# Kernel tuning notes

Measured on AMD Instinct MI355X. Metric: run time of the kernel, lower is better.

Reference implementation:

```python
import jax, jax.numpy as jnp
import numpy as np

D = 2048
H = 16
DK = D // H
B = 2
S = 2048


def setup_inputs() -> dict:
    key = jax.random.key(0)
    ks = jax.random.split(key, 11)
    s = 1.0 / np.sqrt(D)
    inp = {
        "q": jax.random.normal(ks[0], (B, S, D), jnp.float32),
        "k": jax.random.normal(ks[1], (B, S, D), jnp.float32),
        "v": jax.random.normal(ks[2], (B, S, D), jnp.float32),
        "mask": 0,
        "Wq": jax.random.normal(ks[3], (D, D), jnp.float32) * s,
        "bq": jax.random.normal(ks[4], (D,), jnp.float32) * s,
        "Wk": jax.random.normal(ks[5], (D, D), jnp.float32) * s,
        "bk": jax.random.normal(ks[6], (D,), jnp.float32) * s,
        "Wv": jax.random.normal(ks[7], (D, D), jnp.float32) * s,
        "bv": jax.random.normal(ks[8], (D,), jnp.float32) * s,
        "Wo": jax.random.normal(ks[9], (D, D), jnp.float32) * s,
        "bo": jax.random.normal(ks[10], (D,), jnp.float32) * s,
    }
    return inp


def reference(q, k, v, mask, Wq, bq, Wk, bk, Wv, bv, Wo, bo):
    # Linear projections (torch Linear: x @ W.T + b)
    query = q @ Wq.T + bq  # [B,S,D]
    key_ = k @ Wk.T + bk
    value = v @ Wv.T + bv
    # split heads -> [B,S,H,DK]
    query = query.reshape(B, S, H, DK)
    key_ = key_.reshape(B, S, H, DK)
    value = value.reshape(B, S, H, DK)
    # scores [B,H,Sq,Sk]
    scores = jnp.einsum('nqhd,nkhd->nhqk', query, key_)
    if mask:
        # faithful to source: fill where triu(ones, diag=1) == 0 (lower tri incl diag)
        tri = jnp.triu(jnp.ones((S, S), jnp.float32), k=1)
        scores = jnp.where(tri == 0, jnp.float32(-1e20), scores)
    attn = jax.nn.softmax(scores / np.sqrt(DK), axis=3)
    # dropout=0.0 -> identity
    out = jnp.einsum('nhql,nlhd->nqhd', attn, value).reshape(B, S, D)
    return out @ Wo.T + bo
```

## Files before the change

### kernel.cpp

```cpp
#include <hip/hip_runtime.h>
#include <math.h>

typedef unsigned short u16;
typedef u16 u16x8 __attribute__((ext_vector_type(8)));
typedef u16 u16x4 __attribute__((ext_vector_type(4)));
typedef short s16x8 __attribute__((ext_vector_type(8)));
typedef short s16x4 __attribute__((ext_vector_type(4)));
typedef float f32x4 __attribute__((ext_vector_type(4)));

static constexpr int B_ = 2;
static constexpr int S_ = 2048;
static constexpr int D_ = 2048;
static constexpr int H_ = 16;
static constexpr int DK = 128;
static constexpr long long BSD = (long long)B_ * S_ * D_;
static constexpr long long DD  = (long long)D_ * D_;

#if __has_builtin(__builtin_amdgcn_mfma_f32_16x16x32_bf16)
#define HAVE_MFMA32 1
#else
#define HAVE_MFMA32 0
#endif
#if __has_builtin(__builtin_amdgcn_mfma_f32_16x16x16bf16_1k)
#define HAVE_MFMA16 1
#else
#define HAVE_MFMA16 0
#endif

__device__ __forceinline__ u16 f2bf(float f) {
    union { float f; unsigned u; } cv; cv.f = f;
    unsigned u = cv.u;
    return (u16)((u + 0x7fffu + ((u >> 16) & 1u)) >> 16);
}

__device__ __forceinline__ unsigned pack2bf(float a, float b) {
    union { float f; unsigned u; } x, y; x.f = a; y.f = b;
    return ((y.u + 0x8000u) & 0xffff0000u) | ((x.u + 0x8000u) >> 16);
}

__device__ __forceinline__ f32x4 mfma32(f32x4 c, u16x8 a, u16x8 b) {
#if HAVE_MFMA32
    return __builtin_amdgcn_mfma_f32_16x16x32_bf16((s16x8)a, (s16x8)b, c, 0, 0, 0);
#else
    asm volatile("v_mfma_f32_16x16x32_bf16 %0, %1, %2, %0" : "+v"(c) : "v"(a), "v"(b));
    return c;
#endif
}
__device__ __forceinline__ f32x4 mfma16(f32x4 c, u16x4 a, u16x4 b) {
#if HAVE_MFMA16
    return __builtin_amdgcn_mfma_f32_16x16x16bf16_1k((s16x4)a, (s16x4)b, c, 0, 0, 0);
#else
    asm volatile("v_mfma_f32_16x16x16_bf16 %0, %1, %2, %0" : "+v"(c) : "v"(a), "v"(b));
    return c;
#endif
}
__device__ __forceinline__ void fenceB() {
#if !HAVE_MFMA32 || !HAVE_MFMA16
    asm volatile("s_nop 7\ns_nop 7" :::);
#endif
}

__device__ __forceinline__ void glds16(const u16* g, u16* l) {
    __builtin_amdgcn_global_load_lds(
        (const __attribute__((address_space(1))) unsigned int*)g,
        (__attribute__((address_space(3))) unsigned int*)l, 16, 0, 0);
}

__device__ __forceinline__ float fexp2(float x) {
#if __has_builtin(__builtin_amdgcn_exp2f)
    return __builtin_amdgcn_exp2f(x);
#else
    return exp2f(x);
#endif
}

__device__ __forceinline__ void cfence() { asm volatile("" ::: "memory"); }
__device__ __forceinline__ void barrier8() {
    cfence();
    __builtin_amdgcn_s_barrier();
    cfence();
}
#define LGKM0() do { asm volatile("s_waitcnt lgkmcnt(0)" ::: "memory"); \
                     __builtin_amdgcn_sched_barrier(0); } while (0)
#define VMC(N)  asm volatile("s_waitcnt vmcnt(" #N ")" ::: "memory")

struct CastArgs {
    const float* src[7];
    u16* dst[7];
    int start[8];
};
__global__ __launch_bounds__(256) void cast_all(CastArgs a) {
    int g = blockIdx.x * 256 + threadIdx.x;
    if (g >= a.start[7]) return;
    int seg = 0;
#pragma unroll
    for (int i = 1; i < 7; ++i) seg += (g >= a.start[i]) ? 1 : 0;
    int idx = g - a.start[seg];
    float4 f = ((const float4*)a.src[seg])[idx];
    ushort4 o;
    o.x = f2bf(f.x); o.y = f2bf(f.y); o.z = f2bf(f.z); o.w = f2bf(f.w);
    ((ushort4*)a.dst[seg])[idx] = o;
}

#define GEMM_K64_LOOP(Aptr, Bptr)                                                   \
    for (int k0 = 0; k0 < D_; k0 += 64) {                                           \
        __syncthreads();                                                            \
        _Pragma("unroll")                                                           \
        for (int s = 0; s < 4; ++s) {                                               \
            int slot = s * 256 + t;                                                 \
            int row = slot >> 3;                                                    \
            int c = (t & 7) ^ (row & 7);                                            \
            glds16(Aptr + (m0 + row) * D_ + k0 + c * 8, &As[slot * 8]);             \
        }                                                                           \
        _Pragma("unroll")                                                           \
        for (int s = 0; s < 4; ++s) {                                               \
            int slot = s * 256 + t;                                                 \
            int row = slot >> 3;                                                    \
            int c = (t & 7) ^ (row & 7);                                            \
            glds16(Bptr + (n0 + row) * D_ + k0 + c * 8, &Bs[slot * 8]);             \
        }                                                                           \
        __syncthreads();                                                            \
        u16x8 af[4][2], bf[4][2];                                                   \
        _Pragma("unroll")                                                           \
        for (int i = 0; i < 4; ++i) {                                               \
            int row = wm + i * 16 + l16;                                            \
            _Pragma("unroll")                                                       \
            for (int kk = 0; kk < 2; ++kk)                                          \
                af[i][kk] = *(const u16x8*)(&As[row * 64 +                          \
                                (((kk * 4 + quad) ^ (row & 7)) * 8)]);              \
        }                                                                           \
        _Pragma("unroll")                                                           \
        for (int j = 0; j < 4; ++j) {                                               \
            int row = wn + j * 16 + l16;                                            \
            _Pragma("unroll")                                                       \
            for (int kk = 0; kk < 2; ++kk)                                          \
                bf[j][kk] = *(const u16x8*)(&Bs[row * 64 +                          \
                                (((kk * 4 + quad) ^ (row & 7)) * 8)]);              \
        }                                                                           \
        _Pragma("unroll")                                                           \
        for (int kk = 0; kk < 2; ++kk)                                              \
            _Pragma("unroll")                                                       \
            for (int i = 0; i < 4; ++i)                                             \
                _Pragma("unroll")                                                   \
                for (int j = 0; j < 4; ++j)                                         \
                    acc[i][j] = mfma32(acc[i][j], af[i][kk], bf[j][kk]);            \
    }

struct QkvArgs {
    const u16* X[3];
    const u16* W[3];
    const float* bias[3];
    u16* outQ;
    u16* outK;
    u16* outVt;
    float scaleQ;
};

#define STAGE_HALF(LDS, GBASE)                                                      \
    _Pragma("unroll")                                                               \
    for (int jj = 0; jj < 2; ++jj) {                                                \
        int slot = jj * 512 + t;                                                    \
        int row = slot >> 3, c = slot & 7;                                          \
        glds16((GBASE) + (long long)row * D_ + ((c ^ (row & 7)) * 8),               \
               (LDS) + slot * 8);                                                   \
    }

#define RD_A(QM, LDSA)                                                              \
    _Pragma("unroll")                                                               \
    for (int i2 = 0; i2 < 4; ++i2) {                                                \
        int row = wm128 + (QM) * 64 + i2 * 16 + l16;                                \
        _Pragma("unroll")                                                           \
        for (int kk = 0; kk < 2; ++kk)                                              \
            af[(QM) * 4 + i2][kk] = *(const u16x8*)(&(LDSA)[row * 64 +              \
                                (((kk * 4 + quad) ^ (row & 7)) * 8)]);              \
    }

#define RD_B(QN, LDSB)                                                              \
    _Pragma("unroll")                                                               \
    for (int j2 = 0; j2 < 2; ++j2) {                                                \
        int row = wn64 + (QN) * 32 + j2 * 16 + l16;                                 \
        _Pragma("unroll")                                                           \
        for (int kk = 0; kk < 2; ++kk)                                              \
            bf[j2][kk] = *(const u16x8*)(&(LDSB)[row * 64 +                         \
                                (((kk * 4 + quad) ^ (row & 7)) * 8)]);              \
    }

#define MM(QM, QN)                                                                  \
    __builtin_amdgcn_s_setprio(1);                                                  \
    _Pragma("unroll")                                                               \
    for (int kk = 0; kk < 2; ++kk)                                                  \
        _Pragma("unroll")                                                           \
        for (int i2 = 0; i2 < 4; ++i2)                                              \
            _Pragma("unroll")                                                       \
            for (int j2 = 0; j2 < 2; ++j2)                                          \
                acc[(QM) * 4 + i2][(QN) * 2 + j2] =                                 \
                    mfma32(acc[(QM) * 4 + i2][(QN) * 2 + j2],                       \
                           af[(QM) * 4 + i2][kk], bf[j2][kk]);                      \
    __builtin_amdgcn_s_setprio(0);

__global__ __launch_bounds__(512, 2) void qkv_proj8(QkvArgs a) {
    __shared__ u16 SM8[65536];
    u16* const As0 = SM8;
    u16* const As1 = SM8 + 16384;
    u16* const Bs0 = SM8 + 32768;
    u16* const Bs1 = SM8 + 49152;

    const int zsel = blockIdx.z;
    const u16* __restrict__ Ag = a.X[zsel];
    const u16* __restrict__ Bg = a.W[zsel];

    const int t = threadIdx.x;
    const int lane = t & 63;
    const int quad = lane >> 4, l16 = lane & 15;
    const int wave = t >> 6;
    const int wm128 = (wave >> 2) * 128;
    const int wn64  = (wave & 3) * 64;
    const long long m0 = (long long)blockIdx.y * 256;
    const long long n0 = (long long)blockIdx.x * 256;

    f32x4 acc[8][4];
#pragma unroll
    for (int i = 0; i < 8; ++i)
#pragma unroll
        for (int j = 0; j < 4; ++j)
            acc[i][j] = f32x4{0.f, 0.f, 0.f, 0.f};

    u16x8 af[8][2];
    u16x8 bf[2][2];

    STAGE_HALF(As0,         Ag + m0 * D_)
    STAGE_HALF(As0 + 8192,  Ag + (m0 + 128) * D_)
    STAGE_HALF(Bs0,         Bg + n0 * D_)
    STAGE_HALF(Bs0 + 8192,  Bg + (n0 + 128) * D_)
    STAGE_HALF(As1,         Ag + m0 * D_ + 64)
    STAGE_HALF(As1 + 8192,  Ag + (m0 + 128) * D_ + 64)
    VMC(4);
    barrier8();

#pragma unroll 1
    for (int it = 0; it < 16; ++it) {
        const int E = 2 * it;
        const bool more = (it < 15);
        const long long kO  = (long long)(E + 1) * 64;
        const long long kE2 = (long long)(E + 2) * 64;
        const long long kO2 = (long long)(E + 3) * 64;

        RD_A(0, As0) RD_B(0, Bs0)
        STAGE_HALF(Bs1,        Bg + n0 * D_ + kO)
        barrier8(); LGKM0(); MM(0, 0) barrier8();

        RD_A(1, As0) RD_B(1, Bs0)
        STAGE_HALF(Bs1 + 8192, Bg + (n0 + 128) * D_ + kO)
        barrier8(); LGKM0(); MM(0, 1) barrier8();

        RD_B(0, Bs0)
        if (more) { STAGE_HALF(As0,        Ag + m0 * D_ + kE2) }
        barrier8(); LGKM0(); MM(1, 0) barrier8();

        RD_B(1, Bs0)
        if (more) { STAGE_HALF(As0 + 8192, Ag + (m0 + 128) * D_ + kE2) }
        barrier8(); LGKM0(); MM(1, 1)
        if (more) { VMC(4); } else { VMC(0); }
        barrier8();

        RD_A(0, As1) RD_B(0, Bs1)
        if (more) { STAGE_HALF(Bs0,        Bg + n0 * D_ + kE2) }
        barrier8(); LGKM0(); MM(0, 0) barrier8();

        RD_A(1, As1) RD_B(1, Bs1)
        if (more) { STAGE_HALF(Bs0 + 8192, Bg + (n0 + 128) * D_ + kE2) }
        barrier8(); LGKM0(); MM(0, 1) barrier8();

        RD_B(0, Bs1)
        if (more) { STAGE_HALF(As1,        Ag + m0 * D_ + kO2) }
        barrier8(); LGKM0(); MM(1, 0) barrier8();

        RD_B(1, Bs1)
        if (more) { STAGE_HALF(As1 + 8192, Ag + (m0 + 128) * D_ + kO2) }
        barrier8(); LGKM0(); MM(1, 1)
        if (more) { VMC(4); }
        barrier8();
    }
    fenceB();

    float bs[4];
#pragma unroll
    for (int j = 0; j < 4; ++j)
        bs[j] = a.bias[zsel][(int)n0 + wn64 + j * 16 + l16];

    if (zsel < 2) {
        const float scale = (zsel == 0) ? a.scaleQ : 1.0f;
        u16* C = (zsel == 0) ? a.outQ : a.outK;
#pragma unroll
        for (int i = 0; i < 8; ++i)
#pragma unroll
            for (int j = 0; j < 4; ++j)
#pragma unroll
                for (int r = 0; r < 4; ++r) {
                    int row = wm128 + i * 16 + quad * 4 + r;
                    int col = wn64 + j * 16 + l16;
                    SM8[row * 256 + col] = f2bf((acc[i][j][r] + bs[j]) * scale);
                }
        barrier8();
#pragma unroll
        for (int s = 0; s < 16; ++s) {
            int idx = s * 512 + t;
            int row = idx >> 5, c = idx & 31;
            *(u16x8*)(C + (m0 + row) * (long long)D_ + n0 + c * 8) =
                *(const u16x8*)(&SM8[row * 256 + c * 8]);
        }
    } else {
        const int h0 = (int)(n0 >> 7);
        const int bb = (int)(m0 >> 11);
        const int tok0 = (int)(m0 & 2047);
#pragma unroll
        for (int pass = 0; pass < 2; ++pass) {
            barrier8();
            if ((wn64 >> 7) == pass) {
                int cb = wn64 & 127;
#pragma unroll
                for (int i = 0; i < 8; ++i)
#pragma unroll
                    for (int j = 0; j < 4; ++j)
#pragma unroll
                        for (int r = 0; r < 4; ++r) {
                            int row = wm128 + i * 16 + quad * 4 + r;
                            int d = cb + j * 16 + l16;
                            SM8[d * 264 + row] = f2bf(acc[i][j][r] + bs[j]);
                        }
            }
            barrier8();
            u16* vt = a.outVt + (long long)(bb * 16 + h0 + pass) * DK * S_;
#pragma unroll
            for (int s = 0; s < 8; ++s) {
                int idx = s * 512 + t;
                int d = idx >> 5, tc = idx & 31;
                *(u16x8*)(vt + (long long)d * S_ + tok0 + tc * 8) =
                    *(const u16x8*)(&SM8[d * 264 + tc * 8]);
            }
        }
    }
}

__global__ __launch_bounds__(256) void gemm_out(const u16* __restrict__ Ain,
                                                const u16* __restrict__ Bin,
                                                float* __restrict__ C,
                                                const float* __restrict__ bias) {
    __shared__ u16 SM[16384];
    u16* As = SM;
    u16* Bs = SM + 8192;

    const int t = threadIdx.x;
    const int wave = t >> 6, lane = t & 63;
    const int quad = lane >> 4, l16 = lane & 15;
    const int wm = (wave >> 1) * 64;
    const int wn = (wave & 1) * 64;
    const long long m0 = (long long)blockIdx.y * 128;
    const long long n0 = (long long)blockIdx.x * 128;

    f32x4 acc[4][4];
#pragma unroll
    for (int i = 0; i < 4; ++i)
#pragma unroll
        for (int j = 0; j < 4; ++j)
            acc[i][j] = f32x4{0.f, 0.f, 0.f, 0.f};

    GEMM_K64_LOOP(Ain, Bin)

    fenceB();

    float bs[4];
#pragma unroll
    for (int j = 0; j < 4; ++j)
        bs[j] = bias[(int)n0 + wn + j * 16 + l16];

    float* Cf = (float*)SM;
#pragma unroll
    for (int p = 0; p < 2; ++p) {
        __syncthreads();
#pragma unroll
        for (int jj = 0; jj < 2; ++jj) {
            int j = p * 2 + jj;
#pragma unroll
            for (int i = 0; i < 4; ++i)
#pragma unroll
                for (int r = 0; r < 4; ++r) {
                    int row = wm + i * 16 + quad * 4 + r;
                    int lc = (wave & 1) * 32 + jj * 16 + l16;
                    Cf[row * 64 + lc] = acc[i][j][r] + bs[j];
                }
        }
        __syncthreads();
#pragma unroll
        for (int i = 0; i < 8; ++i) {
            int idx = i * 256 + t;
            int row = idx >> 4, c4 = idx & 15;
            f32x4 val = *(const f32x4*)(&Cf[row * 64 + c4 * 4]);
            long long n = n0 + (c4 >> 3) * 64 + p * 32 + (c4 & 7) * 4;
            *(f32x4*)(C + (m0 + row) * (long long)D_ + n) = val;
        }
    }
}

__global__ __launch_bounds__(256, 2) void flash_attn(const u16* __restrict__ Qb,
                                                     const u16* __restrict__ Kb,
                                                     const u16* __restrict__ Vt,
                                                     u16* __restrict__ Ob) {
    __shared__ u16 Ks[2][64 * 128];
    __shared__ u16 Vs[2][128 * 64];

    const int z  = blockIdx.x;
    const int qt = blockIdx.y;
    const int b  = z >> 4, h = z & 15;
    const int t = threadIdx.x, wave = t >> 6, lane = t & 63;
    const int quad = lane >> 4, l16 = lane & 15;

    const u16* kbase = Kb + (long long)(b * S_) * D_ + h * DK;
    const u16* vbase = Vt + (long long)z * DK * S_;

    u16x8 qf[2][4];
    {
        const u16* qbase = Qb + ((long long)(b * S_ + qt * 128 + wave * 32 + l16)) * D_
                              + h * DK + quad * 8;
#pragma unroll
        for (int jq = 0; jq < 2; ++jq)
#pragma unroll
            for (int kk = 0; kk < 4; ++kk)
                qf[jq][kk] = *(const u16x8*)(qbase + (long long)jq * 16 * D_ + kk * 32);
    }

    f32x4 acc_o[2][8];
#pragma unroll
    for (int jq = 0; jq < 2; ++jq)
#pragma unroll
        for (int jd = 0; jd < 8; ++jd)
            acc_o[jq][jd] = f32x4{0.f, 0.f, 0.f, 0.f};
    float l_[2] = {0.f, 0.f};

    u16x8 vreg[4];

    {
#pragma unroll
        for (int i = 0; i < 4; ++i) {
            int slot = i * 256 + t;
            int row = slot >> 3, c16 = slot & 7;
            vreg[i] = *(const u16x8*)(vbase + (long long)row * S_ + c16 * 8);
        }
#pragma unroll
        for (int i = 0; i < 4; ++i) {
            int slot = i * 256 + t;
            int row = slot >> 4;
            int cs = (slot & 15) ^ (row & 7);
            glds16(kbase + (long long)row * D_ + cs * 8, &Ks[0][slot * 8]);
        }
#pragma unroll
        for (int i = 0; i < 4; ++i) {
            int slot = i * 256 + t;
            int row = slot >> 3, c16 = slot & 7;
            int rm = row & 15;
            u16x4 lo = __builtin_shufflevector(vreg[i], vreg[i], 0, 1, 2, 3);
            u16x4 hi = __builtin_shufflevector(vreg[i], vreg[i], 4, 5, 6, 7);
            *(u16x4*)(&Vs[0][row * 64 + (((2 * c16) ^ rm) * 4)]) = lo;
            *(u16x4*)(&Vs[0][row * 64 + (((2 * c16 + 1) ^ rm) * 4)]) = hi;
        }
    }

    for (int kt = 0; kt < S_ / 64; ++kt) {
        __syncthreads();
        const int p = kt & 1;
        const u16* ks = Ks[p];
        const u16* vs = Vs[p];
        const bool pre = (kt + 1) < (S_ / 64);
        if (pre) {
            const u16* vsrc = vbase + (kt + 1) * 64;
#pragma unroll
            for (int i = 0; i < 4; ++i) {
                int slot = i * 256 + t;
                int row = slot >> 3, c16 = slot & 7;
                vreg[i] = *(const u16x8*)(vsrc + (long long)row * S_ + c16 * 8);
            }
            const u16* ksrc = kbase + (long long)(kt + 1) * 64 * D_;
#pragma unroll
            for (int i = 0; i < 4; ++i) {
                int slot = i * 256 + t;
                int row = slot >> 4;
                int cs = (slot & 15) ^ (row & 7);
                glds16(ksrc + (long long)row * D_ + cs * 8, &Ks[p ^ 1][slot * 8]);
            }
        }

        f32x4 st[4][2];
#pragma unroll
        for (int ik = 0; ik < 4; ++ik)
#pragma unroll
            for (int jq = 0; jq < 2; ++jq)
                st[ik][jq] = f32x4{0.f, 0.f, 0.f, 0.f};
#pragma unroll
        for (int kk = 0; kk < 4; ++kk) {
            u16x8 kf[4];
#pragma unroll
            for (int ik = 0; ik < 4; ++ik) {
                int krow = ik * 16 + l16;
                kf[ik] = *(const u16x8*)(&ks[krow * 128 + (((kk * 4 + quad) ^ (l16 & 7)) * 8)]);
            }
#pragma unroll
            for (int ik = 0; ik < 4; ++ik) {
                st[ik][0] = mfma32(st[ik][0], kf[ik], qf[0][kk]);
                st[ik][1] = mfma32(st[ik][1], kf[ik], qf[1][kk]);
            }
        }
        fenceB();

        if (pre) {
#pragma unroll
            for (int i = 0; i < 4; ++i) {
                int slot = i * 256 + t;
                int row = slot >> 3, c16 = slot & 7;
                int rm = row & 15;
                u16x4 lo = __builtin_shufflevector(vreg[i], vreg[i], 0, 1, 2, 3);
                u16x4 hi = __builtin_shufflevector(vreg[i], vreg[i], 4, 5, 6, 7);
                *(u16x4*)(&Vs[p ^ 1][row * 64 + (((2 * c16) ^ rm) * 4)]) = lo;
                *(u16x4*)(&Vs[p ^ 1][row * 64 + (((2 * c16 + 1) ^ rm) * 4)]) = hi;
            }
        }

        u16x4 pf[4][2];
#pragma unroll
        for (int ik = 0; ik < 4; ++ik)
#pragma unroll
            for (int jq = 0; jq < 2; ++jq) {
                float p0 = fexp2(st[ik][jq][0]);
                float p1 = fexp2(st[ik][jq][1]);
                float p2 = fexp2(st[ik][jq][2]);
                float p3 = fexp2(st[ik][jq][3]);
                l_[jq] += (p0 + p1) + (p2 + p3);
                union { u16x4 v; unsigned u[2]; } pk;
                pk.u[0] = pack2bf(p0, p1);
                pk.u[1] = pack2bf(p2, p3);
                pf[ik][jq] = pk.v;
            }

#pragma unroll
        for (int ik = 0; ik < 4; ++ik) {
            const int kc = ik * 4 + quad;
            u16x4 vf[8];
#pragma unroll
            for (int jd = 0; jd < 8; ++jd) {
                int vrow = jd * 16 + l16;
                vf[jd] = *(const u16x4*)(&vs[vrow * 64 + ((kc ^ l16) * 4)]);
            }
#pragma unroll
            for (int jd = 0; jd < 8; ++jd) {
                acc_o[0][jd] = mfma16(acc_o[0][jd], pf[ik][0], vf[jd]);
                acc_o[1][jd] = mfma16(acc_o[1][jd], pf[ik][1], vf[jd]);
            }
        }
        fenceB();
    }

    float lr[2][4];
#pragma unroll
    for (int jq = 0; jq < 2; ++jq) {
        float s = l_[jq];
        s += __shfl_xor(s, 16, 64);
        s += __shfl_xor(s, 32, 64);
        float inv = 1.f / s;
#pragma unroll
        for (int r = 0; r < 4; ++r)
            lr[jq][r] = __shfl(inv, quad * 20 + r, 64);
    }
    u16* OS = (u16*)Ks;
    __syncthreads();
#pragma unroll
    for (int jq = 0; jq < 2; ++jq)
#pragma unroll
        for (int r = 0; r < 4; ++r) {
            int qloc = wave * 32 + jq * 16 + quad * 4 + r;
#pragma unroll
            for (int jd = 0; jd < 8; ++jd)
                OS[qloc * 128 + jd * 16 + l16] = f2bf(acc_o[jq][jd][r] * lr[jq][r]);
        }
    __syncthreads();
    u16* obase = Ob + ((long long)(b * S_ + qt * 128)) * D_ + h * DK;
#pragma unroll
    for (int i = 0; i < 8; ++i) {
        int idx = i * 256 + t;
        int row = idx >> 4, cc = idx & 15;
        *(u16x8*)(obase + (long long)row * D_ + cc * 8) = *(const u16x8*)(&OS[row * 128 + cc * 8]);
    }
}

extern "C" void kernel_launch(void* const* d_in, const int* in_sizes, int n_in,
                              void* d_out, int out_size, void* d_ws, size_t ws_size,
                              hipStream_t stream) {
    const float* q  = (const float*)d_in[0];
    const float* k  = (const float*)d_in[1];
    const float* v  = (const float*)d_in[2];
    const float* Wq = (const float*)d_in[4];
    const float* bq = (const float*)d_in[5];
    const float* Wk = (const float*)d_in[6];
    const float* bk = (const float*)d_in[7];
    const float* Wv = (const float*)d_in[8];
    const float* bv = (const float*)d_in[9];
    const float* Wo = (const float*)d_in[10];
    const float* bo = (const float*)d_in[11];
    float* out = (float*)d_out;

    u16* ws = (u16*)d_ws;
    u16* xq  = ws; ws += BSD;
    u16* xk  = ws; ws += BSD;
    u16* xv  = ws; ws += BSD;
    u16* wqb = ws; ws += DD;
    u16* wkb = ws; ws += DD;
    u16* wvb = ws; ws += DD;
    u16* wob = ws; ws += DD;
    u16* Qb  = ws; ws += BSD;
    u16* Kb  = ws; ws += BSD;
    u16* Vt  = ws; ws += BSD;
    u16* Ob  = ws; ws += BSD;

    const float q_scale = (float)(0.08838834764831845 * 1.4426950408889634);

    {
        CastArgs a;
        const float* srcs[7] = {q, k, v, Wq, Wk, Wv, Wo};
        u16* dsts[7] = {xq, xk, xv, wqb, wkb, wvb, wob};
        int n4s[7] = {(int)(BSD / 4), (int)(BSD / 4), (int)(BSD / 4),
                      (int)(DD / 4), (int)(DD / 4), (int)(DD / 4), (int)(DD / 4)};
        int acc = 0;
        for (int i = 0; i < 7; ++i) { a.src[i] = srcs[i]; a.dst[i] = dsts[i]; a.start[i] = acc; acc += n4s[i]; }
        a.start[7] = acc;
        cast_all<<<(acc + 255) / 256, 256, 0, stream>>>(a);
    }

    {
        QkvArgs a;
        a.X[0] = xq;  a.X[1] = xk;  a.X[2] = xv;
        a.W[0] = wqb; a.W[1] = wkb; a.W[2] = wvb;
        a.bias[0] = bq; a.bias[1] = bk; a.bias[2] = bv;
        a.outQ = Qb; a.outK = Kb; a.outVt = Vt;
        a.scaleQ = q_scale;
        qkv_proj8<<<dim3(D_ / 256, (B_ * S_) / 256, 3), 512, 0, stream>>>(a);
    }

    flash_attn<<<dim3(B_ * H_, S_ / 128), 256, 0, stream>>>(Qb, Kb, Vt, Ob);

    gemm_out<<<dim3(D_ / 128, (B_ * S_) / 128), 256, 0, stream>>>(Ob, wob, out, bo);
}
```

Baseline: 448.8 us.

## Restructure QKV projection into 128x256 tiles with triple-buffered LDS and remapped grid

Replaces the 256x256-tile double-buffered QKV GEMM with a 128x256 tile using a three-slot rotating LDS buffer that stages each K-step's A and B tiles together. The 3D grid becomes a 1D grid of 768 blocks with a custom index swizzle mapping blocks to (z, n, m). Halving the per-block accumulator count lowers register pressure, and the extra blocks give more of them per CU. The aim is better load/compute overlap and occupancy, at the cost of more LDS per block and less data reuse per tile. The V-transpose epilogue is simplified into a single pass.

New measurement: 434.3 us. -3.2%, faster.

```diff
diff --git a/kernel.cpp b/kernel.cpp
--- a/kernel.cpp
+++ b/kernel.cpp
@@ -156,56 +156,50 @@
     float scaleQ;
 };
 
-#define STAGE_HALF(LDS, GBASE)                                                      \
+#define STAGE_U(LDSP, GBASE)                                                        \
     _Pragma("unroll")                                                               \
     for (int jj = 0; jj < 2; ++jj) {                                                \
         int slot = jj * 512 + t;                                                    \
         int row = slot >> 3, c = slot & 7;                                          \
         glds16((GBASE) + (long long)row * D_ + ((c ^ (row & 7)) * 8),               \
-               (LDS) + slot * 8);                                                   \
-    }
-
-#define RD_A(QM, LDSA)                                                              \
+               (LDSP) + slot * 8);                                                  \
+    }
+
+#define RD_K(kk, AsT, BsT)                                                          \
     _Pragma("unroll")                                                               \
     for (int i2 = 0; i2 < 4; ++i2) {                                                \
-        int row = wm128 + (QM) * 64 + i2 * 16 + l16;                                \
-        _Pragma("unroll")                                                           \
-        for (int kk = 0; kk < 2; ++kk)                                              \
-            af[(QM) * 4 + i2][kk] = *(const u16x8*)(&(LDSA)[row * 64 +              \
-                                (((kk * 4 + quad) ^ (row & 7)) * 8)]);              \
-    }
-
-#define RD_B(QN, LDSB)                                                              \
+        int row = wm64 + i2 * 16 + l16;                                             \
+        af2[i2] = *(const u16x8*)(&(AsT)[row * 64 +                                 \
+                        ((((kk) * 4 + quad) ^ (row & 7)) * 8)]);                    \
+    }                                                                               \
     _Pragma("unroll")                                                               \
-    for (int j2 = 0; j2 < 2; ++j2) {                                                \
-        int row = wn64 + (QN) * 32 + j2 * 16 + l16;                                 \
-        _Pragma("unroll")                                                           \
-        for (int kk = 0; kk < 2; ++kk)                                              \
-            bf[j2][kk] = *(const u16x8*)(&(LDSB)[row * 64 +                         \
-                                (((kk * 4 + quad) ^ (row & 7)) * 8)]);              \
-    }
-
-#define MM(QM, QN)                                                                  \
+    for (int j2 = 0; j2 < 4; ++j2) {                                                \
+        int row = wn64 + j2 * 16 + l16;                                             \
+        bf2[j2] = *(const u16x8*)(&(BsT)[row * 64 +                                 \
+                        ((((kk) * 4 + quad) ^ (row & 7)) * 8)]);                    \
+    }
+
+#define MMK()                                                                       \
     __builtin_amdgcn_s_setprio(1);                                                  \
     _Pragma("unroll")                                                               \
-    for (int kk = 0; kk < 2; ++kk)                                                  \
+    for (int i2 = 0; i2 < 4; ++i2)                                                  \
         _Pragma("unroll")                                                           \
-        for (int i2 = 0; i2 < 4; ++i2)                                              \
-            _Pragma("unroll")                                                       \
-            for (int j2 = 0; j2 < 2; ++j2)                                          \
-                acc[(QM) * 4 + i2][(QN) * 2 + j2] =                                 \
-                    mfma32(acc[(QM) * 4 + i2][(QN) * 2 + j2],                       \
-                           af[(QM) * 4 + i2][kk], bf[j2][kk]);                      \
+        for (int j2 = 0; j2 < 4; ++j2)                                              \
+            acc[i2][j2] = mfma32(acc[i2][j2], af2[i2], bf2[j2]);                    \
     __builtin_amdgcn_s_setprio(0);
 
-__global__ __launch_bounds__(512, 2) void qkv_proj8(QkvArgs a) {
-    __shared__ u16 SM8[65536];
-    u16* const As0 = SM8;
-    u16* const As1 = SM8 + 16384;
-    u16* const Bs0 = SM8 + 32768;
-    u16* const Bs1 = SM8 + 49152;
-
-    const int zsel = blockIdx.z;
+__global__ __launch_bounds__(512, 2) void qkv_tri(QkvArgs a) {
+    __shared__ u16 SM8[73728];
+    u16* const Abase = SM8;
+    u16* const Bbase = SM8 + 24576;
+
+    const int l = blockIdx.x;
+    const int f = (l & 7) * 96 + (l >> 3);
+    const int zsel = f >> 8;
+    const int r = f & 255;
+    const int bx = r >> 5;
+    const int by = r & 31;
+
     const u16* __restrict__ Ag = a.X[zsel];
     const u16* __restrict__ Bg = a.W[zsel];
 
@@ -213,73 +207,74 @@
     const int lane = t & 63;
     const int quad = lane >> 4, l16 = lane & 15;
     const int wave = t >> 6;
-    const int wm128 = (wave >> 2) * 128;
-    const int wn64  = (wave & 3) * 64;
-    const long long m0 = (long long)blockIdx.y * 256;
-    const long long n0 = (long long)blockIdx.x * 256;
-
-    f32x4 acc[8][4];
-#pragma unroll
-    for (int i = 0; i < 8; ++i)
+    const int wm64 = (wave >> 2) * 64;
+    const int wn64 = (wave & 3) * 64;
+    const long long m0 = (long long)by * 128;
+    const long long n0 = (long long)bx * 256;
+
+    f32x4 acc[4][4];
+#pragma unroll
+    for (int i = 0; i < 4; ++i)
 #pragma unroll
         for (int j = 0; j < 4; ++j)
             acc[i][j] = f32x4{0.f, 0.f, 0.f, 0.f};
 
-    u16x8 af[8][2];
-    u16x8 bf[2][2];
-
-    STAGE_HALF(As0,         Ag + m0 * D_)
-    STAGE_HALF(As0 + 8192,  Ag + (m0 + 128) * D_)
-    STAGE_HALF(Bs0,         Bg + n0 * D_)
-    STAGE_HALF(Bs0 + 8192,  Bg + (n0 + 128) * D_)
-    STAGE_HALF(As1,         Ag + m0 * D_ + 64)
-    STAGE_HALF(As1 + 8192,  Ag + (m0 + 128) * D_ + 64)
-    VMC(4);
+    u16x8 af2[4], bf2[4];
+
+    STAGE_U(Abase,                Ag + m0 * D_)
+    STAGE_U(Bbase,                Bg + n0 * D_)
+    STAGE_U(Bbase + 8192,         Bg + (n0 + 128) * D_)
+    STAGE_U(Abase + 8192,         Ag + m0 * D_ + 64)
+    STAGE_U(Bbase + 16384,        Bg + n0 * D_ + 64)
+    STAGE_U(Bbase + 16384 + 8192, Bg + (n0 + 128) * D_ + 64)
+    VMC(6);
     barrier8();
 
+    int eb = 0, ob = 1;
 #pragma unroll 1
     for (int it = 0; it < 16; ++it) {
-        const int E = 2 * it;
         const bool more = (it < 15);
-        const long long kO  = (long long)(E + 1) * 64;
-        const long long kE2 = (long long)(E + 2) * 64;
-        const long long kO2 = (long long)(E + 3) * 64;
-
-        RD_A(0, As0) RD_B(0, Bs0)
-        STAGE_HALF(Bs1,        Bg + n0 * D_ + kO)
-        barrier8(); LGKM0(); MM(0, 0) barrier8();
-
-        RD_A(1, As0) RD_B(1, Bs0)
-        STAGE_HALF(Bs1 + 8192, Bg + (n0 + 128) * D_ + kO)
-        barrier8(); LGKM0(); MM(0, 1) barrier8();
-
-        RD_B(0, Bs0)
-        if (more) { STAGE_HALF(As0,        Ag + m0 * D_ + kE2) }
-        barrier8(); LGKM0(); MM(1, 0) barrier8();
-
-        RD_B(1, Bs0)
-        if (more) { STAGE_HALF(As0 + 8192, Ag + (m0 + 128) * D_ + kE2) }
-        barrier8(); LGKM0(); MM(1, 1)
-        if (more) { VMC(4); } else { VMC(0); }
+        const long long kE2 = (long long)(2 * it + 2) * 64;
+        const long long kO2 = kE2 + 64;
+        const int en = (eb + 2 > 2) ? eb - 1 : eb + 2;
+
+        u16* const AsE = Abase + eb * 8192;
+        u16* const BsE = Bbase + eb * 16384;
+        u16* const AsO = Abase + ob * 8192;
+        u16* const BsO = Bbase + ob * 16384;
+        u16* const AsnE = Abase + en * 8192;
+        u16* const BsnE = Bbase + en * 16384;
+        u16* const AsnO = AsE;
+        u16* const BsnO = BsE;
+
+        RD_K(0, AsE, BsE)
+        if (more) {
+            STAGE_U(AsnE, Ag + m0 * D_ + kE2)
+            STAGE_U(BsnE, Bg + n0 * D_ + kE2)
+        }
+        barrier8(); LGKM0(); MMK() barrier8();
+
+        RD_K(1, AsE, BsE)
+        if (more) { STAGE_U(BsnE + 8192, Bg + (n0 + 128) * D_ + kE2) }
+        barrier8(); LGKM0(); MMK()
+        if (more) { VMC(6); } else { VMC(0); }
         barrier8();
 
-        RD_A(0, As1) RD_B(0, Bs1)
-        if (more) { STAGE_HALF(Bs0,        Bg + n0 * D_ + kE2) }
-        barrier8(); LGKM0(); MM(0, 0) barrier8();
-
-        RD_A(1, As1) RD_B(1, Bs1)
-        if (more) { STAGE_HALF(Bs0 + 8192, Bg + (n0 + 128) * D_ + kE2) }
-        barrier8(); LGKM0(); MM(0, 1) barrier8();
-
-        RD_B(0, Bs1)
-        if (more) { STAGE_HALF(As1,        Ag + m0 * D_ + kO2) }
-        barrier8(); LGKM0(); MM(1, 0) barrier8();
-
-        RD_B(1, Bs1)
-        if (more) { STAGE_HALF(As1 + 8192, Ag + (m0 + 128) * D_ + kO2) }
-        barrier8(); LGKM0(); MM(1, 1)
-        if (more) { VMC(4); }
+        RD_K(0, AsO, BsO)
+        if (more) {
+            STAGE_U(AsnO, Ag + m0 * D_ + kO2)
+            STAGE_U(BsnO, Bg + n0 * D_ + kO2)
+        }
+        barrier8(); LGKM0(); MMK() barrier8();
+
+        RD_K(1, AsO, BsO)
+        if (more) { STAGE_U(BsnO + 8192, Bg + (n0 + 128) * D_ + kO2) }
+        barrier8(); LGKM0(); MMK()
+        if (more) { VMC(6); }
         barrier8();
+
+        eb = en;
+        ob = (ob + 2 > 2) ? ob - 1 : ob + 2;
     }
     fenceB();
 
@@ -292,18 +287,18 @@
         const float scale = (zsel == 0) ? a.scaleQ : 1.0f;
         u16* C = (zsel == 0) ? a.outQ : a.outK;
 #pragma unroll
-        for (int i = 0; i < 8; ++i)
+        for (int i = 0; i < 4; ++i)
 #pragma unroll
             for (int j = 0; j < 4; ++j)
 #pragma unroll
-                for (int r = 0; r < 4; ++r) {
-                    int row = wm128 + i * 16 + quad * 4 + r;
+                for (int rr = 0; rr < 4; ++rr) {
+                    int row = wm64 + i * 16 + quad * 4 + rr;
                     int col = wn64 + j * 16 + l16;
-                    SM8[row * 256 + col] = f2bf((acc[i][j][r] + bs[j]) * scale);
+                    SM8[row * 256 + col] = f2bf((acc[i][j][rr] + bs[j]) * scale);
                 }
         barrier8();
 #pragma unroll
-        for (int s = 0; s < 16; ++s) {
+        for (int s = 0; s < 8; ++s) {
             int idx = s * 512 + t;
             int row = idx >> 5, c = idx & 31;
             *(u16x8*)(C + (m0 + row) * (long long)D_ + n0 + c * 8) =
@@ -314,29 +309,25 @@
         const int bb = (int)(m0 >> 11);
         const int tok0 = (int)(m0 & 2047);
 #pragma unroll
-        for (int pass = 0; pass < 2; ++pass) {
-            barrier8();
-            if ((wn64 >> 7) == pass) {
-                int cb = wn64 & 127;
-#pragma unroll
-                for (int i = 0; i < 8; ++i)
-#pragma unroll
-                    for (int j = 0; j < 4; ++j)
-#pragma unroll
-                        for (int r = 0; r < 4; ++r) {
-                            int row = wm128 + i * 16 + quad * 4 + r;
-                            int d = cb + j * 16 + l16;
-                            SM8[d * 264 + row] = f2bf(acc[i][j][r] + bs[j]);
-                        }
-            }
-            barrier8();
-            u16* vt = a.outVt + (long long)(bb * 16 + h0 + pass) * DK * S_;
-#pragma unroll
-            for (int s = 0; s < 8; ++s) {
+        for (int i = 0; i < 4; ++i)
+#pragma unroll
+            for (int j = 0; j < 4; ++j)
+#pragma unroll
+                for (int rr = 0; rr < 4; ++rr) {
+                    int row = wm64 + i * 16 + quad * 4 + rr;
+                    int d = wn64 + j * 16 + l16;
+                    SM8[d * 136 + row] = f2bf(acc[i][j][rr] + bs[j]);
+                }
+        barrier8();
+#pragma unroll
+        for (int hh = 0; hh < 2; ++hh) {
+            u16* vt = a.outVt + (long long)(bb * 16 + h0 + hh) * DK * S_;
+#pragma unroll
+            for (int s = 0; s < 4; ++s) {
                 int idx = s * 512 + t;
-                int d = idx >> 5, tc = idx & 31;
+                int d = idx >> 4, tc = idx & 15;
                 *(u16x8*)(vt + (long long)d * S_ + tok0 + tc * 8) =
-                    *(const u16x8*)(&SM8[d * 264 + tc * 8]);
+                    *(const u16x8*)(&SM8[(hh * 128 + d) * 136 + tc * 8]);
             }
         }
     }
@@ -640,7 +631,7 @@
         a.bias[0] = bq; a.bias[1] = bk; a.bias[2] = bv;
         a.outQ = Qb; a.outK = Kb; a.outVt = Vt;
         a.scaleQ = q_scale;
-        qkv_proj8<<<dim3(D_ / 256, (B_ * S_) / 256, 3), 512, 0, stream>>>(a);
+        qkv_tri<<<dim3(768, 1, 1), 512, 0, stream>>>(a);
     }
 
     flash_attn<<<dim3(B_ * H_, S_ / 128), 256, 0, stream>>>(Qb, Kb, Vt, Ob);
```
